# Kernel optimization log

Hardware: AMD Instinct MI355X
Metric: run time of the kernel (lower is better)

Reference implementation:

```python
import jax, jax.numpy as jnp
import numpy as np

B, C_IN, C_OUT, T = 128, 256, 512, 200
H, K = 8, 64
KS, DIL = 3, 2
PAD = (KS - 1) * DIL  # causal left padding


def setup_inputs() -> dict:
    key = jax.random.key(0)
    ks = jax.random.split(key, 14)
    s = 0.02
    return {
        "x": jax.random.normal(ks[0], (B, C_IN, T), jnp.float32),
        "Wq": jax.random.normal(ks[1], (C_IN, H * K), jnp.float32) * s,
        "bq": jnp.zeros((H * K,), jnp.float32),
        "Wk": jax.random.normal(ks[2], (C_IN, H * K), jnp.float32) * s,
        "bk": jnp.zeros((H * K,), jnp.float32),
        "Wv": jax.random.normal(ks[3], (C_IN, H * C_IN), jnp.float32) * s,
        "bv": jnp.zeros((H * C_IN,), jnp.float32),
        "Wp": jax.random.normal(ks[4], (H * C_IN, C_IN), jnp.float32) * s,
        "bp": jnp.zeros((C_IN,), jnp.float32),
        "Wc": jax.random.normal(ks[5], (C_OUT, C_IN, KS), jnp.float32) * s,
        "bc": jnp.zeros((C_OUT,), jnp.float32),
        "Wd": jax.random.normal(ks[6], (C_OUT, C_IN, 1), jnp.float32) * s,
        "bd": jnp.zeros((C_OUT,), jnp.float32),
    }


def reference(x, Wq, bq, Wk, bk, Wv, bv, Wp, bp, Wc, bc, Wd, bd):
    xp = jnp.transpose(x, (0, 2, 1))  # (B,T,C)
    q = (xp @ Wq + bq).reshape(B, T, H, K).transpose(0, 2, 1, 3)       # (B,H,T,K)
    k = (xp @ Wk + bk).reshape(B, T, H, K).transpose(0, 2, 1, 3)       # (B,H,T,K)
    v = (xp @ Wv + bv).reshape(B, T, H, C_IN).transpose(0, 2, 1, 3)    # (B,H,T,C)
    scores = jnp.einsum("bhtk,bhsk->bhts", q, k) / np.sqrt(K).astype(jnp.float32)
    mask = jnp.tril(jnp.ones((T, T), bool))
    scores = jnp.where(mask, scores, -jnp.inf)
    att = jax.nn.softmax(scores, axis=-1)                               # (B,H,T,T)
    y = jnp.einsum("bhts,bhsc->bhtc", att, v)                           # (B,H,T,C)
    y = y.transpose(0, 2, 1, 3).reshape(B, T, H * C_IN)
    attn_out = (y @ Wp + bp).transpose(0, 2, 1)                         # (B,C,T)
    conv = jax.lax.conv_general_dilated(
        attn_out, Wc, window_strides=(1,), padding=[(PAD, 0)],
        rhs_dilation=(DIL,), dimension_numbers=("NCH", "OIH", "NCH"))
    conv = jax.nn.relu(conv + bc[None, :, None])                        # (B,C_OUT,T)
    res = jnp.einsum("oi,bit->bot", Wd[:, :, 0], x) + bd[None, :, None]
    return jax.nn.relu(conv + res), att
```

## Files before the change

### kernel.cpp

```cpp
#include <hip/hip_runtime.h>
#include <hip/hip_bf16.h>
#include <math.h>

#define BB 128
#define CIN 256
#define COUT 512
#define TT 200
#define HH 8
#define KD 64
#define HK 512
#define HC 2048
#define QR 56

typedef __hip_bfloat16 bf16;
typedef __attribute__((ext_vector_type(8))) short s16x8;
typedef __attribute__((ext_vector_type(4))) short s16x4;
typedef __attribute__((ext_vector_type(4))) float f32x4;

#define MFMA(a, b, c) __builtin_amdgcn_mfma_f32_16x16x32_bf16(a, b, c, 0, 0, 0)

__device__ __forceinline__ short bfs(float f) {
  bf16 h = __float2bfloat16(f);
  return *reinterpret_cast<short*>(&h);
}
__device__ __forceinline__ s16x8 ld8(const bf16* p) {
  return *reinterpret_cast<const s16x8*>(p);
}

__global__ __launch_bounds__(256) void k_xb(const float* __restrict__ x, bf16* __restrict__ xb,
                                            bf16* __restrict__ xtb) {
  __shared__ float lx[CIN][33];
  int blk = blockIdx.x, b = blk / 7, tt = blk % 7, t0 = tt * 32;
  int tid = threadIdx.x;
  const float* xbp = x + (size_t)b * CIN * TT;
  bf16* xo = xb + (size_t)b * 208 * CIN;
  bf16* xto = xtb + (size_t)b * CIN * 224;
  for (int idx = tid; idx < CIN * 32; idx += 256) {
    int c = idx >> 5, tl = idx & 31, t = t0 + tl;
    lx[c][tl] = (t < TT) ? xbp[(size_t)c * TT + t] : 0.f;
  }
  __syncthreads();
  for (int idx = tid; idx < CIN * 32; idx += 256) {
    int c = idx >> 5, tl = idx & 31;
    xto[(size_t)c * 224 + t0 + tl] = __float2bfloat16(lx[c][tl]);
  }
  for (int idx = tid; idx < 32 * 64; idx += 256) {
    int tl = idx >> 6, cs = idx & 63, t = t0 + tl;
    if (t < TT) {
      s16x4 p;
      p[0] = bfs(lx[cs * 4 + 0][tl]); p[1] = bfs(lx[cs * 4 + 1][tl]);
      p[2] = bfs(lx[cs * 4 + 2][tl]); p[3] = bfs(lx[cs * 4 + 3][tl]);
      *reinterpret_cast<s16x4*>(&xo[(size_t)t * CIN + cs * 4]) = p;
    }
  }
  if (tt == 6) {
    s16x4 z = {0, 0, 0, 0};
    for (int idx = tid; idx < 8 * 64; idx += 256) {
      int r = 200 + (idx >> 6), cs = idx & 63;
      *reinterpret_cast<s16x4*>(&xo[(size_t)r * CIN + cs * 4]) = z;
    }
  }
}

__global__ __launch_bounds__(256) void k_wc(const float* __restrict__ Wc,
    const float* __restrict__ Wd, bf16* __restrict__ Wcb, bf16* __restrict__ Wdb) {
  int o = blockIdx.x, i = threadIdx.x;
  size_t oi = (size_t)o * CIN + i;
#pragma unroll
  for (int j = 0; j < 3; ++j)
    Wcb[(size_t)j * COUT * CIN + oi] = __float2bfloat16(Wc[oi * 3 + j]);
  Wdb[oi] = __float2bfloat16(Wd[oi]);
}

__global__ __launch_bounds__(256) void k_wqk(const float* __restrict__ Wq,
    const float* __restrict__ Wk, bf16* __restrict__ WqT, bf16* __restrict__ WkT) {
  int n = blockIdx.x, ci = threadIdx.x;
  WqT[(size_t)n * CIN + ci] = __float2bfloat16(Wq[(size_t)ci * HK + n]);
  WkT[(size_t)n * CIN + ci] = __float2bfloat16(Wk[(size_t)ci * HK + n]);
}

__global__ __launch_bounds__(256) void k_wvp(const float* __restrict__ Wv,
    const float* __restrict__ Wp, const float* __restrict__ bv,
    bf16* __restrict__ WvpT, float* __restrict__ bvp) {
  __shared__ __align__(16) float wpl[32][256];
  __shared__ __align__(16) float wvl[17][32];
  int h = blockIdx.x >> 4, ci0 = (blockIdx.x & 15) << 4;
  int c = threadIdx.x;
  float acc[17];
#pragma unroll
  for (int i = 0; i < 17; ++i) acc[i] = 0.f;
  for (int p0 = 0; p0 < CIN; p0 += 32) {
    __syncthreads();
    for (int idx = c; idx < 17 * 32; idx += 256) {
      int pp = idx & 31, cil = idx >> 5;
      wvl[cil][pp] = (cil < 16) ? Wv[(size_t)(ci0 + cil) * HC + h * CIN + p0 + pp]
                                : bv[h * CIN + p0 + pp];
    }
    for (int idx = c; idx < 32 * 256; idx += 256) {
      int cc = idx & 255, pp = idx >> 8;
      wpl[pp][cc] = Wp[(size_t)(h * CIN + p0 + pp) * CIN + cc];
    }
    __syncthreads();
#pragma unroll 4
    for (int pp = 0; pp < 32; ++pp) {
      float w = wpl[pp][c];
#pragma unroll
      for (int i = 0; i < 17; ++i) acc[i] += wvl[i][pp] * w;
    }
  }
  for (int i = 0; i < 16; ++i)
    WvpT[((size_t)h * CIN + c) * CIN + ci0 + i] = __float2bfloat16(acc[i]);
  if (ci0 == 0) bvp[h * CIN + c] = acc[16];
}

__global__ __launch_bounds__(256) void k_qk(const bf16* __restrict__ xb,
    const bf16* __restrict__ WqT, const bf16* __restrict__ WkT,
    const float* __restrict__ bq, const float* __restrict__ bk,
    bf16* __restrict__ qo, bf16* __restrict__ kvo) {
  int blk = blockIdx.x, b = blk & 127, quad = blk >> 7;
  int tid = threadIdx.x, w = tid >> 6, l = tid & 63;
  int lrow = l & 15, g = l >> 4;
  int cw = quad * 64 + w * 16 + lrow;
  const bf16* xbb = xb + (size_t)b * 208 * CIN;
  const bf16* wqt = WqT + (size_t)cw * CIN;
  const bf16* wkt = WkT + (size_t)cw * CIN;
  f32x4 aq[13], ak[13];
#pragma unroll
  for (int mt = 0; mt < 13; ++mt) {
    aq[mt] = (f32x4){0.f, 0.f, 0.f, 0.f};
    ak[mt] = (f32x4){0.f, 0.f, 0.f, 0.f};
  }
  for (int kc = 0; kc < 8; ++kc) {
    int kof = kc * 32 + g * 8;
    s16x8 bqf = ld8(&wqt[kof]);
    s16x8 bkf = ld8(&wkt[kof]);
#pragma unroll
    for (int mt = 0; mt < 13; ++mt) {
      s16x8 afr = ld8(&xbb[(size_t)(mt * 16 + lrow) * CIN + kof]);
      aq[mt] = MFMA(afr, bqf, aq[mt]);
      ak[mt] = MFMA(afr, bkf, ak[mt]);
    }
  }
  float bqv = bq[cw], bkv = bk[cw];
#pragma unroll
  for (int mt = 0; mt < 13; ++mt) {
#pragma unroll
    for (int r = 0; r < 4; ++r) {
      int t = mt * 16 + g * 4 + r;
      if (t < TT) {
        qo[((size_t)b * TT + t) * HK + cw] = __float2bfloat16(aq[mt][r] + bqv);
        kvo[((size_t)b * TT + t) * HK + cw] = __float2bfloat16(ak[mt][r] + bkv);
      }
    }
  }
}

__global__ __launch_bounds__(256) void k_attn(const bf16* __restrict__ qo,
    const bf16* __restrict__ kvo, float* __restrict__ att) {
  int bh = blockIdx.x, b = bh >> 3, h = bh & 7;
  int tid = threadIdx.x, w = tid >> 6, l = tid & 63;
  int lrow = l & 15, g = l >> 4;
  const bf16* qb = qo + (size_t)b * TT * HK + h * KD;
  const bf16* kb = kvo + (size_t)b * TT * HK + h * KD;
  float* ab = att + (size_t)bh * TT * TT;
  for (int mt = w; mt < 13; mt += 4) {
    int ra = mt * 16 + lrow; if (ra > TT - 1) ra = TT - 1;
    s16x8 a0 = ld8(&qb[(size_t)ra * HK + g * 8]);
    s16x8 a1 = ld8(&qb[(size_t)ra * HK + 32 + g * 8]);
    f32x4 sacc[13];
#pragma unroll
    for (int st = 0; st < 13; ++st) sacc[st] = (f32x4){0.f, 0.f, 0.f, 0.f};
#pragma unroll
    for (int st = 0; st < 13; ++st) {
      if (st <= mt) {
        int rb = st * 16 + lrow; if (rb > TT - 1) rb = TT - 1;
        s16x8 b0 = ld8(&kb[(size_t)rb * HK + g * 8]);
        s16x8 b1 = ld8(&kb[(size_t)rb * HK + 32 + g * 8]);
        sacc[st] = MFMA(a0, b0, sacc[st]);
        sacc[st] = MFMA(a1, b1, sacc[st]);
      }
    }
#pragma unroll
    for (int r = 0; r < 4; ++r) {
      int m = mt * 16 + g * 4 + r;
      if (m >= TT) continue;
      float vals[13];
      float mx = -INFINITY;
#pragma unroll
      for (int st = 0; st < 13; ++st) {
        int col = st * 16 + lrow;
        float v = sacc[st][r] * 0.125f;
        vals[st] = (st <= mt && col <= m) ? v : -INFINITY;
        mx = fmaxf(mx, vals[st]);
      }
#pragma unroll
      for (int off = 1; off < 16; off <<= 1) mx = fmaxf(mx, __shfl_xor(mx, off));
      float e[13], sum = 0.f;
#pragma unroll
      for (int st = 0; st < 13; ++st) {
        e[st] = (vals[st] > -INFINITY) ? __expf(vals[st] - mx) : 0.f;
        sum += e[st];
      }
#pragma unroll
      for (int off = 1; off < 16; off <<= 1) sum += __shfl_xor(sum, off);
      float inv = 1.f / sum;
#pragma unroll
      for (int st = 0; st < 13; ++st) {
        int col = st * 16 + lrow;
        if (col < TT) ab[(size_t)m * TT + col] = e[st] * inv;
      }
    }
  }
}

__global__ __launch_bounds__(512) void k_avx(const float* __restrict__ att,
    const bf16* __restrict__ xtb, const bf16* __restrict__ WvpT,
    const float* __restrict__ bvp, const float* __restrict__ bp,
    bf16* __restrict__ atTp) {
  __shared__ short satt[64 * 232];
  __shared__ short yl[64 * 260];
  int blk = blockIdx.x, b = blk & 127, q = blk >> 7;
  int t0 = q * QR;
  int tid = threadIdx.x, w = tid >> 6, l = tid & 63;
  int lrow = l & 15, g = l >> 4;
  bf16* atb = atTp + (size_t)b * 216 * CIN;
  bf16 zb = __float2bfloat16(0.f);
  if (q == 0) { for (int idx = tid; idx < 4 * CIN; idx += 512) atb[idx] = zb; }
  if (q == 3) { for (int idx = tid; idx < 8 * CIN; idx += 512) atb[204 * CIN + idx] = zb; }
  const bf16* xr = xtb + (size_t)b * CIN * 224;
  int ns = (t0 + QR - 1) / 32 + 1; if (ns > 7) ns = 7;
  int srow = tid >> 3, scid = tid & 7;
  int sra = t0 + srow; if (sra > TT - 1) sra = TT - 1;
  const float* srcrow;
  f32x4 acc2[4][2];
#pragma unroll
  for (int mt = 0; mt < 4; ++mt)
#pragma unroll
    for (int nt = 0; nt < 2; ++nt) acc2[mt][nt] = (f32x4){0.f, 0.f, 0.f, 0.f};
  for (int h = 0; h < HH; ++h) {
    const float* abh = att + (size_t)(b * HH + h) * TT * TT;
    srcrow = abh + (size_t)sra * TT;
    __syncthreads();
    for (int jj = 0; jj < ns; ++jj) {
      int ch = jj * 8 + scid;
      int col = ch * 4;
      float4 v = {0.f, 0.f, 0.f, 0.f};
      if (col < TT) v = *(const float4*)&srcrow[col];
      s16x4 p;
      p[0] = bfs(v.x); p[1] = bfs(v.y); p[2] = bfs(v.z); p[3] = bfs(v.w);
      *reinterpret_cast<s16x4*>(&satt[srow * 232 + ch * 4]) = p;
    }
    __syncthreads();
    f32x4 acc1[2][4];
#pragma unroll
    for (int mc = 0; mc < 2; ++mc)
#pragma unroll
      for (int nt = 0; nt < 4; ++nt) acc1[mc][nt] = (f32x4){0.f, 0.f, 0.f, 0.f};
    for (int s0 = 0; s0 < ns * 32; s0 += 32) {
      s16x8 bat[4];
#pragma unroll
      for (int nt = 0; nt < 4; ++nt)
        bat[nt] = *reinterpret_cast<const s16x8*>(&satt[(nt * 16 + lrow) * 232 + s0 + g * 8]);
#pragma unroll
      for (int mc = 0; mc < 2; ++mc) {
        s16x8 af = ld8(&xr[(size_t)(w * 32 + mc * 16 + lrow) * 224 + s0 + g * 8]);
#pragma unroll
        for (int nt = 0; nt < 4; ++nt)
          acc1[mc][nt] = MFMA(af, bat[nt], acc1[mc][nt]);
      }
    }
    __syncthreads();
#pragma unroll
    for (int mc = 0; mc < 2; ++mc)
#pragma unroll
      for (int nt = 0; nt < 4; ++nt) {
        s16x4 p;
        p[0] = bfs(acc1[mc][nt][0]); p[1] = bfs(acc1[mc][nt][1]);
        p[2] = bfs(acc1[mc][nt][2]); p[3] = bfs(acc1[mc][nt][3]);
        *reinterpret_cast<s16x4*>(&yl[(nt * 16 + lrow) * 260 + w * 32 + mc * 16 + g * 4]) = p;
      }
    __syncthreads();
    const bf16* wv = WvpT + (size_t)h * CIN * CIN;
#pragma unroll
    for (int kc = 0; kc < 8; ++kc) {
      int kof = kc * 32 + g * 8;
      s16x8 bw[2];
#pragma unroll
      for (int nt = 0; nt < 2; ++nt)
        bw[nt] = ld8(&wv[(size_t)(w * 32 + nt * 16 + lrow) * CIN + kof]);
#pragma unroll
      for (int mt = 0; mt < 4; ++mt) {
        s16x4 alo = *reinterpret_cast<const s16x4*>(&yl[(mt * 16 + lrow) * 260 + kof]);
        s16x4 ahi = *reinterpret_cast<const s16x4*>(&yl[(mt * 16 + lrow) * 260 + kof + 4]);
        s16x8 ay;
        ay[0] = alo[0]; ay[1] = alo[1]; ay[2] = alo[2]; ay[3] = alo[3];
        ay[4] = ahi[0]; ay[5] = ahi[1]; ay[6] = ahi[2]; ay[7] = ahi[3];
#pragma unroll
        for (int nt = 0; nt < 2; ++nt)
          acc2[mt][nt] = MFMA(ay, bw[nt], acc2[mt][nt]);
      }
    }
  }
  int climit = TT - t0; if (climit > QR) climit = QR;
#pragma unroll
  for (int nt = 0; nt < 2; ++nt) {
    int c = w * 32 + nt * 16 + lrow;
    float bsum = bp[c];
#pragma unroll
    for (int h = 0; h < HH; ++h) bsum += bvp[h * CIN + c];
#pragma unroll
    for (int mt = 0; mt < 4; ++mt) {
#pragma unroll
      for (int r = 0; r < 4; ++r) {
        int tloc = mt * 16 + g * 4 + r;
        if (tloc < climit)
          atb[(size_t)(t0 + tloc + 4) * CIN + c] = __float2bfloat16(acc2[mt][nt][r] + bsum);
      }
    }
  }
}

__global__ __launch_bounds__(256) void k_conv(const bf16* __restrict__ atTp,
    const bf16* __restrict__ xb, const bf16* __restrict__ Wcb, const bf16* __restrict__ Wdb,
    const float* __restrict__ bc, const float* __restrict__ bd, float* __restrict__ out0) {
  __shared__ short satb[116 * 64];
  __shared__ short sxb[112 * 64];
  int blk = blockIdx.x, b = blk & 127, og = (blk >> 7) & 7, th = blk >> 10;
  int t0 = th * 100;
  int tid = threadIdx.x, w = tid >> 6, l = tid & 63;
  int lrow = l & 15, g = l >> 4;
  int o0 = og * 64 + w * 16;
  const bf16* wc0 = Wcb + (size_t)(o0 + lrow) * CIN;
  const bf16* wc1 = wc0 + (size_t)COUT * CIN;
  const bf16* wc2 = wc1 + (size_t)COUT * CIN;
  const bf16* wdp = Wdb + (size_t)(o0 + lrow) * CIN;
  const bf16* atb = atTp + (size_t)b * 216 * CIN;
  const bf16* xbb = xb + (size_t)b * 208 * CIN;
  f32x4 accc[7], accr[7];
#pragma unroll
  for (int nt = 0; nt < 7; ++nt) {
    accc[nt] = (f32x4){0.f, 0.f, 0.f, 0.f};
    accr[nt] = (f32x4){0.f, 0.f, 0.f, 0.f};
  }
  s16x8 pa[4], px[4];
  const s16x8 z8 = {0, 0, 0, 0, 0, 0, 0, 0};
#pragma unroll
  for (int j = 0; j < 4; ++j) {
    int idx = tid + j * 256;
    pa[j] = z8; px[j] = z8;
    if (idx < 116 * 8) pa[j] = ld8(&atb[(size_t)(t0 + (idx >> 3)) * CIN + (idx & 7) * 8]);
    if (idx < 112 * 8) {
      int gx = t0 + (idx >> 3); if (gx > 207) gx = 207;
      px[j] = ld8(&xbb[(size_t)gx * CIN + (idx & 7) * 8]);
    }
  }
  for (int ks = 0; ks < 4; ++ks) {
    int kb0 = ks * 64;
    __syncthreads();
#pragma unroll
    for (int j = 0; j < 4; ++j) {
      int idx = tid + j * 256;
      if (idx < 116 * 8) {
        int row = idx >> 3, ch = idx & 7;
        *reinterpret_cast<s16x8*>(&satb[row * 64 + ((ch ^ (row & 7)) * 8)]) = pa[j];
      }
      if (idx < 112 * 8) {
        int row = idx >> 3, ch = idx & 7;
        *reinterpret_cast<s16x8*>(&sxb[row * 64 + ((ch ^ (row & 7)) * 8)]) = px[j];
      }
    }
    if (ks < 3) {
      int kb1 = kb0 + 64;
#pragma unroll
      for (int j = 0; j < 4; ++j) {
        int idx = tid + j * 256;
        if (idx < 116 * 8) pa[j] = ld8(&atb[(size_t)(t0 + (idx >> 3)) * CIN + kb1 + (idx & 7) * 8]);
        if (idx < 112 * 8) {
          int gx = t0 + (idx >> 3); if (gx > 207) gx = 207;
          px[j] = ld8(&xbb[(size_t)gx * CIN + kb1 + (idx & 7) * 8]);
        }
      }
    }
    __syncthreads();
#pragma unroll
    for (int kcl = 0; kcl < 2; ++kcl) {
      int kof = kb0 + kcl * 32 + g * 8;
      s16x8 a0 = ld8(&wc0[kof]);
      s16x8 a1 = ld8(&wc1[kof]);
      s16x8 a2 = ld8(&wc2[kof]);
      s16x8 ad = ld8(&wdp[kof]);
      int chb = kcl * 4 + g;
#pragma unroll
      for (int nt = 0; nt < 7; ++nt) {
        int r0 = nt * 16 + lrow, r1 = r0 + 2, r2 = r0 + 4;
        s16x8 b0 = *reinterpret_cast<const s16x8*>(&satb[r0 * 64 + ((chb ^ (r0 & 7)) * 8)]);
        s16x8 b1 = *reinterpret_cast<const s16x8*>(&satb[r1 * 64 + ((chb ^ (r1 & 7)) * 8)]);
        s16x8 b2 = *reinterpret_cast<const s16x8*>(&satb[r2 * 64 + ((chb ^ (r2 & 7)) * 8)]);
        s16x8 bx = *reinterpret_cast<const s16x8*>(&sxb[r0 * 64 + ((chb ^ (r0 & 7)) * 8)]);
        accc[nt] = MFMA(a0, b0, accc[nt]);
        accc[nt] = MFMA(a1, b1, accc[nt]);
        accc[nt] = MFMA(a2, b2, accc[nt]);
        accr[nt] = MFMA(ad, bx, accr[nt]);
      }
    }
  }
  f32x4 bcv = *reinterpret_cast<const f32x4*>(&bc[o0 + g * 4]);
  f32x4 bdv = *reinterpret_cast<const f32x4*>(&bd[o0 + g * 4]);
#pragma unroll
  for (int nt = 0; nt < 7; ++nt) {
    int tloc = nt * 16 + lrow;
    if (tloc < 100) {
      int t = t0 + tloc;
#pragma unroll
      for (int r = 0; r < 4; ++r) {
        int o = o0 + g * 4 + r;
        float conv = fmaxf(accc[nt][r] + bcv[r], 0.f);
        out0[((size_t)b * COUT + o) * TT + t] = fmaxf(conv + accr[nt][r] + bdv[r], 0.f);
      }
    }
  }
}

extern "C" void kernel_launch(void* const* d_in, const int* in_sizes, int n_in,
                              void* d_out, int out_size, void* d_ws, size_t ws_size,
                              hipStream_t stream) {
  const float* x  = (const float*)d_in[0];
  const float* Wq = (const float*)d_in[1];
  const float* bq = (const float*)d_in[2];
  const float* Wk = (const float*)d_in[3];
  const float* bk = (const float*)d_in[4];
  const float* Wv = (const float*)d_in[5];
  const float* bv = (const float*)d_in[6];
  const float* Wp = (const float*)d_in[7];
  const float* bp = (const float*)d_in[8];
  const float* Wc = (const float*)d_in[9];
  const float* bc = (const float*)d_in[10];
  const float* Wd = (const float*)d_in[11];
  const float* bd = (const float*)d_in[12];

  float* out0 = (float*)d_out;
  float* att  = out0 + (size_t)BB * COUT * TT;

  char* ws = (char*)d_ws;
  bf16*  qo   = (bf16*)(ws);
  bf16*  atTp = (bf16*)(ws);
  bf16*  kvo  = (bf16*)(ws + 26214400);
  bf16*  xtb  = (bf16*)(ws + 52428800);
  bf16*  xb   = (bf16*)(ws + 157286400);
  bf16*  WvpT = (bf16*)(ws + 170917888);
  float* bvp  = (float*)(ws + 171966464);
  bf16*  Wcb  = (bf16*)(ws + 171974656);
  bf16*  Wdb  = (bf16*)(ws + 172761088);
  bf16*  WqT  = (bf16*)(ws + 173023232);
  bf16*  WkT  = (bf16*)(ws + 173285376);

  hipLaunchKernelGGL(k_wvp,  dim3(128),      dim3(256), 0, stream, Wv, Wp, bv, WvpT, bvp);
  hipLaunchKernelGGL(k_wc,   dim3(COUT),     dim3(256), 0, stream, Wc, Wd, Wcb, Wdb);
  hipLaunchKernelGGL(k_wqk,  dim3(HK),       dim3(256), 0, stream, Wq, Wk, WqT, WkT);
  hipLaunchKernelGGL(k_xb,   dim3(BB * 7),   dim3(256), 0, stream, x, xb, xtb);
  hipLaunchKernelGGL(k_qk,   dim3(BB * 8),   dim3(256), 0, stream, xb, WqT, WkT, bq, bk, qo, kvo);
  hipLaunchKernelGGL(k_attn, dim3(BB * HH),  dim3(256), 0, stream, qo, kvo, att);
  hipLaunchKernelGGL(k_avx,  dim3(BB * 4),   dim3(512), 0, stream, att, xtb, WvpT, bvp, bp, atTp);
  hipLaunchKernelGGL(k_conv, dim3(BB * 16),  dim3(256), 0, stream, atTp, xb, Wcb, Wdb, bc, bd, out0);
}
```

Before: 368.6 us.

## Balance causal attention-V work by pairing short and long row blocks per CTA

Replaces the four contiguous 56-row query chunks in k_avx with pairs of 32-row blocks (r and 5-r), plus a lone final 8-row block, so each CTA processes a similar total causal length. Each half of the tile loads and multiplies only over its own key-range count. The aim is to remove load imbalance from the causal triangle, where the last chunk did most of the work. In exchange there is branchy per-half MFMA logic, and the p==3 CTA uses only 8 valid rows of a 64-row tile.

```diff
diff --git a/kernel.cpp b/kernel.cpp
--- a/kernel.cpp
+++ b/kernel.cpp
@@ -10,7 +10,6 @@
 #define KD 64
 #define HK 512
 #define HC 2048
-#define QR 56
 
 typedef __hip_bfloat16 bf16;
 typedef __attribute__((ext_vector_type(8))) short s16x8;
@@ -219,36 +218,41 @@
     bf16* __restrict__ atTp) {
   __shared__ short satt[64 * 232];
   __shared__ short yl[64 * 260];
-  int blk = blockIdx.x, b = blk & 127, q = blk >> 7;
-  int t0 = q * QR;
+  int blk = blockIdx.x, b = blk & 127, p = blk >> 7;
+  bool hasB = (p < 3);
+  int rA = hasB ? p : 6, rB = 5 - p;
+  int nsA = rA + 1, nsB = rB + 1;
+  int nsTot = hasB ? nsB : nsA;
   int tid = threadIdx.x, w = tid >> 6, l = tid & 63;
   int lrow = l & 15, g = l >> 4;
   bf16* atb = atTp + (size_t)b * 216 * CIN;
   bf16 zb = __float2bfloat16(0.f);
-  if (q == 0) { for (int idx = tid; idx < 4 * CIN; idx += 512) atb[idx] = zb; }
-  if (q == 3) { for (int idx = tid; idx < 8 * CIN; idx += 512) atb[204 * CIN + idx] = zb; }
+  if (p == 0) { for (int idx = tid; idx < 4 * CIN; idx += 512) atb[idx] = zb; }
+  if (p == 3) { for (int idx = tid; idx < 8 * CIN; idx += 512) atb[204 * CIN + idx] = zb; }
   const bf16* xr = xtb + (size_t)b * CIN * 224;
-  int ns = (t0 + QR - 1) / 32 + 1; if (ns > 7) ns = 7;
   int srow = tid >> 3, scid = tid & 7;
-  int sra = t0 + srow; if (sra > TT - 1) sra = TT - 1;
-  const float* srcrow;
+  int sT = (srow < 32) ? (rA * 32 + srow) : (rB * 32 + (srow - 32));
+  if (sT > TT - 1) sT = TT - 1;
+  int snrow = (srow < 32) ? nsA : nsB;
+  bool sact = (srow < 32) || hasB;
   f32x4 acc2[4][2];
 #pragma unroll
   for (int mt = 0; mt < 4; ++mt)
 #pragma unroll
     for (int nt = 0; nt < 2; ++nt) acc2[mt][nt] = (f32x4){0.f, 0.f, 0.f, 0.f};
   for (int h = 0; h < HH; ++h) {
-    const float* abh = att + (size_t)(b * HH + h) * TT * TT;
-    srcrow = abh + (size_t)sra * TT;
-    __syncthreads();
-    for (int jj = 0; jj < ns; ++jj) {
-      int ch = jj * 8 + scid;
-      int col = ch * 4;
-      float4 v = {0.f, 0.f, 0.f, 0.f};
-      if (col < TT) v = *(const float4*)&srcrow[col];
-      s16x4 p;
-      p[0] = bfs(v.x); p[1] = bfs(v.y); p[2] = bfs(v.z); p[3] = bfs(v.w);
-      *reinterpret_cast<s16x4*>(&satt[srow * 232 + ch * 4]) = p;
+    const float* srcrow = att + (size_t)(b * HH + h) * TT * TT + (size_t)sT * TT;
+    __syncthreads();
+    if (sact) {
+      for (int jj = 0; jj < snrow; ++jj) {
+        int ch = jj * 8 + scid;
+        int col = ch * 4;
+        float4 v = {0.f, 0.f, 0.f, 0.f};
+        if (col < TT) v = *(const float4*)&srcrow[col];
+        s16x4 pk;
+        pk[0] = bfs(v.x); pk[1] = bfs(v.y); pk[2] = bfs(v.z); pk[3] = bfs(v.w);
+        *reinterpret_cast<s16x4*>(&satt[srow * 232 + ch * 4]) = pk;
+      }
     }
     __syncthreads();
     f32x4 acc1[2][4];
@@ -256,17 +260,25 @@
     for (int mc = 0; mc < 2; ++mc)
 #pragma unroll
       for (int nt = 0; nt < 4; ++nt) acc1[mc][nt] = (f32x4){0.f, 0.f, 0.f, 0.f};
-    for (int s0 = 0; s0 < ns * 32; s0 += 32) {
-      s16x8 bat[4];
-#pragma unroll
-      for (int nt = 0; nt < 4; ++nt)
-        bat[nt] = *reinterpret_cast<const s16x8*>(&satt[(nt * 16 + lrow) * 232 + s0 + g * 8]);
-#pragma unroll
-      for (int mc = 0; mc < 2; ++mc) {
-        s16x8 af = ld8(&xr[(size_t)(w * 32 + mc * 16 + lrow) * 224 + s0 + g * 8]);
-#pragma unroll
-        for (int nt = 0; nt < 4; ++nt)
-          acc1[mc][nt] = MFMA(af, bat[nt], acc1[mc][nt]);
+    for (int ss = 0; ss < nsTot; ++ss) {
+      int s0 = ss * 32;
+      s16x8 af0 = ld8(&xr[(size_t)(w * 32 + lrow) * 224 + s0 + g * 8]);
+      s16x8 af1 = ld8(&xr[(size_t)(w * 32 + 16 + lrow) * 224 + s0 + g * 8]);
+      if (ss < nsA) {
+        s16x8 b0 = *reinterpret_cast<const s16x8*>(&satt[(lrow) * 232 + s0 + g * 8]);
+        s16x8 b1 = *reinterpret_cast<const s16x8*>(&satt[(16 + lrow) * 232 + s0 + g * 8]);
+        acc1[0][0] = MFMA(af0, b0, acc1[0][0]);
+        acc1[0][1] = MFMA(af0, b1, acc1[0][1]);
+        acc1[1][0] = MFMA(af1, b0, acc1[1][0]);
+        acc1[1][1] = MFMA(af1, b1, acc1[1][1]);
+      }
+      if (hasB && ss < nsB) {
+        s16x8 b2 = *reinterpret_cast<const s16x8*>(&satt[(32 + lrow) * 232 + s0 + g * 8]);
+        s16x8 b3 = *reinterpret_cast<const s16x8*>(&satt[(48 + lrow) * 232 + s0 + g * 8]);
+        acc1[0][2] = MFMA(af0, b2, acc1[0][2]);
+        acc1[0][3] = MFMA(af0, b3, acc1[0][3]);
+        acc1[1][2] = MFMA(af1, b2, acc1[1][2]);
+        acc1[1][3] = MFMA(af1, b3, acc1[1][3]);
       }
     }
     __syncthreads();
@@ -274,10 +286,10 @@
     for (int mc = 0; mc < 2; ++mc)
 #pragma unroll
       for (int nt = 0; nt < 4; ++nt) {
-        s16x4 p;
-        p[0] = bfs(acc1[mc][nt][0]); p[1] = bfs(acc1[mc][nt][1]);
-        p[2] = bfs(acc1[mc][nt][2]); p[3] = bfs(acc1[mc][nt][3]);
-        *reinterpret_cast<s16x4*>(&yl[(nt * 16 + lrow) * 260 + w * 32 + mc * 16 + g * 4]) = p;
+        s16x4 pk;
+        pk[0] = bfs(acc1[mc][nt][0]); pk[1] = bfs(acc1[mc][nt][1]);
+        pk[2] = bfs(acc1[mc][nt][2]); pk[3] = bfs(acc1[mc][nt][3]);
+        *reinterpret_cast<s16x4*>(&yl[(nt * 16 + lrow) * 260 + w * 32 + mc * 16 + g * 4]) = pk;
       }
     __syncthreads();
     const bf16* wv = WvpT + (size_t)h * CIN * CIN;
@@ -301,7 +313,6 @@
       }
     }
   }
-  int climit = TT - t0; if (climit > QR) climit = QR;
 #pragma unroll
   for (int nt = 0; nt < 2; ++nt) {
     int c = w * 32 + nt * 16 + lrow;
@@ -313,8 +324,11 @@
 #pragma unroll
       for (int r = 0; r < 4; ++r) {
         int tloc = mt * 16 + g * 4 + r;
-        if (tloc < climit)
-          atb[(size_t)(t0 + tloc + 4) * CIN + c] = __float2bfloat16(acc2[mt][nt][r] + bsum);
+        int tg_; bool valid;
+        if (tloc < 32) { tg_ = rA * 32 + tloc; valid = hasB || (tloc < 8); }
+        else           { tg_ = rB * 32 + (tloc - 32); valid = hasB; }
+        if (valid)
+          atb[(size_t)(tg_ + 4) * CIN + c] = __float2bfloat16(acc2[mt][nt][r] + bsum);
       }
     }
   }
```

New measurement: 365.2 us. About the same (-0.9%).
